# Performance work log

Hardware: AMD Instinct MI355X
Metric: run time of the kernel (lower is better)

## Reference

```python
import jax, jax.numpy as jnp
import numpy as np

D = 64          # graph size d
HID = 1024      # hidden_dim of drift/diffusion MLPs


def _mlp(A_flat, t_val, W1, b1, W2, b2):
    """MLP over flattened adjacency concatenated with scalar time. A_flat: (..., d*d)."""
    t_col = jnp.full(A_flat.shape[:-1] + (1,), t_val, dtype=A_flat.dtype)
    x = jnp.concatenate([A_flat, t_col], axis=-1)          # (..., d*d+1)
    h = jnp.tanh(x @ W1 + b1)                              # (..., HID)
    return h @ W2 + b2                                     # (..., d*d)


def setup_inputs() -> dict:
    key = jax.random.key(0)
    ks = jax.random.split(key, 12)
    B, T = 64, 64
    A0 = jax.random.normal(ks[0], (B, D, D), dtype=jnp.float32)
    t = jnp.arange(T, dtype=jnp.float32) * 0.01
    din = D * D + 1
    s1 = 1.0 / np.sqrt(din)
    s2 = 1.0 / np.sqrt(HID)
    W1f = jax.random.normal(ks[1], (din, HID), jnp.float32) * s1
    b1f = jnp.zeros((HID,), jnp.float32)
    W2f = jax.random.normal(ks[2], (HID, D * D), jnp.float32) * s2
    b2f = jnp.zeros((D * D,), jnp.float32)
    W1g = jax.random.normal(ks[3], (din, HID), jnp.float32) * s1
    b1g = jnp.zeros((HID,), jnp.float32)
    W2g = jax.random.normal(ks[4], (HID, D * D), jnp.float32) * s2
    b2g = jnp.zeros((D * D,), jnp.float32)
    return dict(A0=A0, t=t, W1f=W1f, b1f=b1f, W2f=W2f, b2f=b2f,
                W1g=W1g, b1g=b1g, W2g=W2g, b2g=b2g, num_samples=4)


def reference(A0, t, W1f, b1f, W2f, b2f, W1g, b1g, W2g, b2g, num_samples):
    S = num_samples
    B = A0.shape[0]
    T = t.shape[0]
    dt = t[1] - t[0]
    sqrt_dt = jnp.sqrt(dt)
    A_init = jnp.broadcast_to(A0[None], (S, B, D, D))
    noise_keys = jax.random.split(jax.random.key(42), T - 1)

    def step(A_prev, inp):
        t_prev, k = inp
        Af = A_prev.reshape(S, B, D * D)
        drift = _mlp(Af, t_prev, W1f, b1f, W2f, b2f).reshape(S, B, D, D)
        diffusion = jax.nn.softplus(_mlp(Af, t_prev, W1g, b1g, W2g, b2g)).reshape(S, B, D, D)
        # torch draws dW with shape (*batch, d, d): shared across num_samples
        dW = jax.random.normal(k, (B, D, D), dtype=A_prev.dtype) * sqrt_dt
        A_next = A_prev + drift * dt + diffusion * dW
        return A_next, A_next

    _, traj = jax.lax.scan(step, A_init, (t[:-1], noise_keys))   # (T-1, S, B, d, d)
    A = jnp.concatenate([A_init[None], traj], axis=0)            # (T, S, B, d, d)
    A = jnp.swapaxes(A, 0, 1)                                    # (S, T, B, d, d)
    # ThresholdedSigmoid in training mode + zeroed diagonal
    G = jax.nn.sigmoid(A) * (1.0 - jnp.eye(D, dtype=A.dtype))
    return G
```

## Files before the change

kernel.cpp:

```cpp
#include <hip/hip_runtime.h>
#include <cstdint>

using u16 = unsigned short;
using u32 = uint32_t;
using u64 = unsigned long long;

typedef __bf16 bf16x8 __attribute__((ext_vector_type(8)));
typedef float  f32x4  __attribute__((ext_vector_type(4)));
typedef u32    uvec4  __attribute__((ext_vector_type(4)));

typedef const __attribute__((address_space(1))) void GV;
typedef __attribute__((address_space(3))) void LV;

#define MFMA(a, b, c) __builtin_amdgcn_mfma_f32_16x16x32_bf16((a), (b), (c), 0, 0, 0)
#define SCOPE_AGT __HIP_MEMORY_SCOPE_AGENT

static __device__ __forceinline__ void gl_lds16(const u16* g, u16* l) {
  __builtin_amdgcn_global_load_lds((GV*)g, (LV*)l, 16, 0, 0);
}
static __device__ __forceinline__ void st_dev(u64* p, u64 v) {
  __hip_atomic_store(p, v, __ATOMIC_RELAXED, SCOPE_AGT);
}
static __device__ __forceinline__ void wait_tags(const u32* ctr, int base, u32 tag) {
  const int lane = threadIdx.x & 63;
  const u32* p = ctr + (size_t)(base + (lane & 31)) * 32;
  u32 v = __hip_atomic_load(p, __ATOMIC_RELAXED, SCOPE_AGT);
  while (!__all(v >= tag)) {
    __builtin_amdgcn_s_sleep(4);
    v = __hip_atomic_load(p, __ATOMIC_RELAXED, SCOPE_AGT);
  }
  asm volatile("" ::: "memory");
}

static __device__ __forceinline__ u16 f2bf(float x) {
  u32 u = __float_as_uint(x);
  u32 r = (u + 0x7FFFu + ((u >> 16) & 1u)) >> 16;
  return (u16)r;
}

static __device__ __forceinline__ u32 rotl32(u32 v, int s) {
  return (v << s) | (v >> (32 - s));
}

static __device__ __forceinline__ void threefry2x32(u32 k0, u32 k1, u32 x0, u32 x1,
                                                    u32& o0, u32& o1) {
  u32 k2 = k0 ^ k1 ^ 0x1BD11BDAu;
  x0 += k0; x1 += k1;
  x0 += x1; x1 = rotl32(x1, 13); x1 ^= x0;
  x0 += x1; x1 = rotl32(x1, 15); x1 ^= x0;
  x0 += x1; x1 = rotl32(x1, 26); x1 ^= x0;
  x0 += x1; x1 = rotl32(x1, 6);  x1 ^= x0;
  x0 += k1; x1 += k2 + 1u;
  x0 += x1; x1 = rotl32(x1, 17); x1 ^= x0;
  x0 += x1; x1 = rotl32(x1, 29); x1 ^= x0;
  x0 += x1; x1 = rotl32(x1, 16); x1 ^= x0;
  x0 += x1; x1 = rotl32(x1, 24); x1 ^= x0;
  x0 += k2; x1 += k0 + 2u;
  x0 += x1; x1 = rotl32(x1, 13); x1 ^= x0;
  x0 += x1; x1 = rotl32(x1, 15); x1 ^= x0;
  x0 += x1; x1 = rotl32(x1, 26); x1 ^= x0;
  x0 += x1; x1 = rotl32(x1, 6);  x1 ^= x0;
  x0 += k0; x1 += k1 + 3u;
  x0 += x1; x1 = rotl32(x1, 17); x1 ^= x0;
  x0 += x1; x1 = rotl32(x1, 29); x1 ^= x0;
  x0 += x1; x1 = rotl32(x1, 16); x1 ^= x0;
  x0 += x1; x1 = rotl32(x1, 24); x1 ^= x0;
  x0 += k1; x1 += k2 + 4u;
  x0 += x1; x1 = rotl32(x1, 13); x1 ^= x0;
  x0 += x1; x1 = rotl32(x1, 15); x1 ^= x0;
  x0 += x1; x1 = rotl32(x1, 26); x1 ^= x0;
  x0 += x1; x1 = rotl32(x1, 6);  x1 ^= x0;
  x0 += k2; x1 += k0 + 5u;
  o0 = x0; o1 = x1;
}

static __device__ __forceinline__ float bits_to_normal(u32 bits) {
  const float lo = __uint_as_float(0xBF7FFFFFu);
  float f = __uint_as_float((bits >> 9) | 0x3F800000u) - 1.0f;
  float x = fmaxf(lo, f * 2.0f + lo);
  float w = -logf((1.0f - x) * (1.0f + x));
  float p;
  if (w < 5.0f) {
    w -= 2.5f;
    p = 2.81022636e-08f;
    p = fmaf(p, w, 3.43273939e-07f);
    p = fmaf(p, w, -3.5233877e-06f);
    p = fmaf(p, w, -4.39150654e-06f);
    p = fmaf(p, w, 0.00021858087f);
    p = fmaf(p, w, -0.00125372503f);
    p = fmaf(p, w, -0.00417768164f);
    p = fmaf(p, w, 0.246640727f);
    p = fmaf(p, w, 1.50140941f);
  } else {
    w = sqrtf(w) - 3.0f;
    p = -0.000200214257f;
    p = fmaf(p, w, 0.000100950558f);
    p = fmaf(p, w, 0.00134934322f);
    p = fmaf(p, w, -0.00367342844f);
    p = fmaf(p, w, 0.00573950773f);
    p = fmaf(p, w, -0.0076224613f);
    p = fmaf(p, w, 0.00943887047f);
    p = fmaf(p, w, 1.00167406f);
    p = fmaf(p, w, 2.83297682f);
  }
  return 1.41421356f * p * x;
}

__global__ __launch_bounds__(256) void s1_frag(
    const float* __restrict__ W1f, const float* __restrict__ W1g,
    const float* __restrict__ W2f, const float* __restrict__ W2g,
    u16* __restrict__ W1P, u16* __restrict__ W2P) {
  const int gid = blockIdx.x * 256 + threadIdx.x;
  const int f = gid >> 6, l = gid & 63;
  const int lr = l & 15, kg = l >> 4;
  u32 wbuf[4];
  if (f < 16384) {
    const int net = f >> 13, r = f & 8191, ct = r >> 7, q = r & 127;
    const float* __restrict__ src = net ? W1g : W1f;
    const int k = q * 32 + kg * 8, c = ct * 16 + lr;
    #pragma unroll
    for (int p = 0; p < 4; ++p) {
      u16 e0 = f2bf(src[(size_t)(k + 2 * p) * 1024 + c]);
      u16 e1 = f2bf(src[(size_t)(k + 2 * p + 1) * 1024 + c]);
      wbuf[p] = (u32)e0 | ((u32)e1 << 16);
    }
    *(uvec4*)(W1P + (size_t)f * 512 + l * 8) = *(uvec4*)wbuf;
  } else {
    const int f2 = f - 16384;
    const int net = f2 >> 13, r = f2 & 8191, ct = r >> 5, q = r & 31;
    const float* __restrict__ src = net ? W2g : W2f;
    const int k = q * 32 + kg * 8, c = ct * 16 + lr;
    #pragma unroll
    for (int p = 0; p < 4; ++p) {
      u16 e0 = f2bf(src[(size_t)(k + 2 * p) * 4096 + c]);
      u16 e1 = f2bf(src[(size_t)(k + 2 * p + 1) * 4096 + c]);
      wbuf[p] = (u32)e0 | ((u32)e1 << 16);
    }
    *(uvec4*)(W2P + (size_t)f2 * 512 + l * 8) = *(uvec4*)wbuf;
  }
}

__global__ __launch_bounds__(256) void s2_init(
    const float* __restrict__ A0, u16* __restrict__ APack,
    u32* __restrict__ ctr, float* __restrict__ out) {
  const int gid = blockIdx.x * 256 + threadIdx.x;
  const int n = gid & 4095, b = gid >> 12;
  const float a0 = A0[gid];
  const float sig = (n % 65 == 0) ? 0.0f : 1.0f / (1.0f + expf(-a0));
  #pragma unroll
  for (int s = 0; s < 4; ++s)
    out[((size_t)(s * 64) * 64 + b) * 4096 + n] = sig;
  if (gid < 32768) {
    const int fr = gid >> 6, l = gid & 63;
    const int m = fr >> 7, q = fr & 127;
    const int row = m * 16 + (l & 15);
    const int k = q * 32 + (l >> 4) * 8;
    u32 wbuf[4];
    #pragma unroll
    for (int p = 0; p < 4; ++p) {
      u16 e0 = f2bf(A0[(size_t)row * 4096 + k + 2 * p]);
      u16 e1 = f2bf(A0[(size_t)row * 4096 + k + 2 * p + 1]);
      wbuf[p] = (u32)e0 | ((u32)e1 << 16);
    }
    *(uvec4*)(APack + (size_t)fr * 512 + l * 8) = *(uvec4*)wbuf;
  }
  if (gid < 16640) ctr[gid] = 0;
}

__global__ __launch_bounds__(512, 2) void sde_fused(
    const float* __restrict__ A0, const float* __restrict__ tarr,
    const u16* __restrict__ W1P, const u16* __restrict__ W2P,
    const float* __restrict__ b1f, const float* __restrict__ b1g,
    const float* __restrict__ W1fv, const float* __restrict__ W1gv,
    const float* __restrict__ b2f, const float* __restrict__ b2g,
    u16* __restrict__ APack, u16* __restrict__ HPack,
    u32* __restrict__ ctr, float* __restrict__ out) {
  extern __shared__ __align__(16) char smraw[];
  u16* w2l = (u16*)smraw;
  char* exraw = smraw + 131072;
  f32x4 (*paex)[64]     = (f32x4 (*)[64])exraw;
  u16 (*patile)[16][16] = (u16 (*)[16][16])(exraw + 8192);
  f32x4 (*pbex)[64][2]  = (f32x4 (*)[64][2])exraw;
  u16 (*pbtile)[16][32] = (u16 (*)[16][32])(exraw + 16384);
  uint2* dwk = (uint2*)(exraw + 18432);

  const int bid = blockIdx.x, tix = threadIdx.x;
  const int wid = tix >> 6, lane = tix & 63;
  const int lr = lane & 15, lq = lane >> 4;
  const int mp = bid >> 7;
  const int ctF = bid & 127;
  const int netA = ctF >> 6, ctA = ctF & 63;
  const int mA = wid & 1, ksA = wid >> 1;
  const int mGA = mp * 2 + mA;
  const int ct32 = bid & 127;
  const int ksB = wid >> 2, netB = (wid >> 1) & 1, mB = wid & 1;
  const int mGB = mp * 2 + mB;
  const int eM = wid & 1, eCf = (wid >> 1) & 1, eRh = wid >> 2;
  const int nc = ct32 * 32 + eCf * 16 + lr;

  u32* tagA = ctr + (size_t)bid * 32;
  u32* tagB = ctr + (size_t)(256 + bid) * 32;
  const int waitAbase = 256 + mp * 128 + ksA * 32;
  const int waitBbase = mp * 128 + netB * 64 + ksB * 32;

  #pragma unroll
  for (int i = 0; i < 16; ++i) {
    const int f = wid * 16 + i;
    const int nf = f >> 6, cf = (f >> 5) & 1, ksf = (f >> 4) & 1, df = f & 15;
    const u16* src = W2P
        + ((size_t)((nf * 256 + ct32 * 2 + cf) * 32 + ksf * 16 + df)) * 512 + lane * 8;
    gl_lds16(src, w2l + (size_t)f * 512);
  }
  if (tix < 63) {
    u32 y0, y1;
    threefry2x32(0u, 42u, 0u, (u32)tix, y0, y1);
    dwk[tix] = make_uint2(y0, y1);
  }
  bf16x8 wv[32];
  {
    const u16* pw = W1P + ((size_t)((netA * 64 + ctA) * 128 + ksA * 32)) * 512 + lane * 8;
    #pragma unroll
    for (int d = 0; d < 32; ++d) wv[d] = *(const bf16x8*)(pw + (size_t)d * 512);
  }
  float Ast[2];
  #pragma unroll
  for (int ri = 0; ri < 2; ++ri) {
    const int row = mp * 32 + eM * 16 + lq * 4 + eRh * 2 + ri;
    Ast[ri] = A0[(size_t)row * 4096 + nc];
  }
  const int nclA = ctA * 16 + lr;
  const float bAc = (netA ? b1g : b1f)[nclA];
  const float wAc = ((netA ? W1gv : W1fv) + (size_t)4096 * 1024)[nclA];
  const float bfv = b2f[nc], bgv = b2g[nc];
  const bool diag0 = (nc % 65 == 0);
  asm volatile("s_waitcnt vmcnt(0)" ::: "memory");
  __syncthreads();

  const float dt = tarr[1] - tarr[0];
  const float sdt = sqrtf(dt);

  for (int step = 0; step < 63; ++step) {
    const u32 tag = (u32)step + 1u;
    {
      wait_tags(ctr, waitAbase, (u32)step);
      const u16* pa = APack + (size_t)step * 262144
                    + ((size_t)(mGA * 128 + ksA * 32)) * 512 + lane * 8;
      bf16x8 av[16];
      #pragma unroll
      for (int d = 0; d < 16; ++d) av[d] = *(const bf16x8*)(pa + (size_t)d * 512);
      f32x4 acc0 = {0.f, 0.f, 0.f, 0.f}, acc1 = acc0;
      #pragma unroll
      for (int j = 0; j < 32; ++j) {
        const int s = j & 15;
        if (j & 1) acc1 = MFMA(av[s], wv[j], acc1);
        else       acc0 = MFMA(av[s], wv[j], acc0);
        if (j + 16 < 32) av[s] = *(const bf16x8*)(pa + (size_t)(j + 16) * 512);
      }
      paex[wid][lane] = acc0 + acc1;
      __syncthreads();
      {
        const int gM = wid & 1, gR = wid >> 1;
        const f32x4 s0 = paex[gM][lane];
        const f32x4 s1 = paex[2 + gM][lane];
        const f32x4 s2 = paex[4 + gM][lane];
        const f32x4 s3 = paex[6 + gM][lane];
        const float ch = s0[gR] + s1[gR] + s2[gR] + s3[gR];
        const float cc = bAc + tarr[step] * wAc;
        patile[gM][lq * 4 + gR][lr] = f2bf(tanhf(ch + cc));
      }
      __syncthreads();
      if (wid < 2 && lane < 32) {
        const int mm = wid;
        const int row = lane & 15, kp = lane >> 4;
        const u16* src = &patile[mm][row][kp * 8];
        const u64 lo = *(const u64*)src;
        const u64 hi = *(const u64*)(src + 4);
        const int k8 = (ctA & 1) * 2 + kp;
        u16* dst = HPack + (size_t)step * 131072
                 + ((size_t)((netA * 4 + mp * 2 + mm) * 32 + (ctA >> 1))) * 512
                 + (k8 * 16 + row) * 8;
        st_dev((u64*)dst, lo);
        st_dev((u64*)dst + 1, hi);
      }
      asm volatile("s_waitcnt vmcnt(0)" ::: "memory");
      __syncthreads();
      if (tix == 0)
        __hip_atomic_store(tagA, tag, __ATOMIC_RELAXED, SCOPE_AGT);
    }

    {
      wait_tags(ctr, waitBbase, tag);
      const u16* ph = HPack + (size_t)step * 131072
                    + ((size_t)((netB * 4 + mGB) * 32 + ksB * 16)) * 512 + lane * 8;
      bf16x8 hv[16];
      #pragma unroll
      for (int d = 0; d < 16; ++d) hv[d] = *(const bf16x8*)(ph + (size_t)d * 512);
      const u16* wl0 = w2l + (size_t)(netB * 64 + ksB * 16) * 512 + lane * 8;
      const u16* wl1 = wl0 + (size_t)32 * 512;
      f32x4 a0 = {0.f, 0.f, 0.f, 0.f}, a1 = a0;
      #pragma unroll
      for (int j = 0; j < 16; ++j) {
        const bf16x8 w0 = *(const bf16x8*)(wl0 + (size_t)j * 512);
        const bf16x8 w1 = *(const bf16x8*)(wl1 + (size_t)j * 512);
        a0 = MFMA(hv[j], w0, a0);
        a1 = MFMA(hv[j], w1, a1);
      }
      pbex[wid][lane][0] = a0;
      pbex[wid][lane][1] = a1;
      __syncthreads();
      float sg[2];
      {
        const f32x4 CF = pbex[eM][lane][eCf] + pbex[4 + eM][lane][eCf];
        const f32x4 CG = pbex[2 + eM][lane][eCf] + pbex[6 + eM][lane][eCf];
        const uint2 key = dwk[step];
        #pragma unroll
        for (int ri = 0; ri < 2; ++ri) {
          const int r = eRh * 2 + ri;
          const int row = mp * 32 + eM * 16 + lq * 4 + r;
          const float drift = CF[r] + bfv;
          const float graw = CG[r] + bgv;
          const float diff = fmaxf(graw, 0.0f) + log1pf(expf(-fabsf(graw)));
          u32 y0, y1;
          threefry2x32(key.x, key.y, 0u, (u32)(row * 4096 + nc), y0, y1);
          const float dw = bits_to_normal(y0 ^ y1) * sdt;
          const float an = Ast[ri] + drift * dt + diff * dw;
          Ast[ri] = an;
          pbtile[eM][lq * 4 + r][eCf * 16 + lr] = f2bf(an);
          sg[ri] = diag0 ? 0.0f : 1.0f / (1.0f + expf(-an));
        }
      }
      __syncthreads();
      if (wid < 2) {
        const int mm = wid;
        const int row = lane & 15, kq = lane >> 4;
        const u16* src = &pbtile[mm][row][kq * 8];
        const u64 lo = *(const u64*)src;
        const u64 hi = *(const u64*)(src + 4);
        u16* dst = APack + (size_t)(step + 1) * 262144
                 + ((size_t)((mp * 2 + mm) * 128 + ct32)) * 512 + lane * 8;
        st_dev((u64*)dst, lo);
        st_dev((u64*)dst + 1, hi);
      }
      asm volatile("s_waitcnt vmcnt(0)" ::: "memory");
      __syncthreads();
      if (tix == 0)
        __hip_atomic_store(tagB, tag, __ATOMIC_RELAXED, SCOPE_AGT);
      #pragma unroll
      for (int ri = 0; ri < 2; ++ri) {
        const int row = mp * 32 + eM * 16 + lq * 4 + eRh * 2 + ri;
        #pragma unroll
        for (int s = 0; s < 4; ++s)
          __builtin_nontemporal_store(
              sg[ri], &out[((size_t)(s * 64 + step + 1) * 64 + row) * 4096 + nc]);
      }
    }
  }
}

extern "C" void kernel_launch(void* const* d_in, const int* in_sizes, int n_in,
                              void* d_out, int out_size, void* d_ws, size_t ws_size,
                              hipStream_t stream) {
  const float* A0 = (const float*)d_in[0];
  const float* tarr = (const float*)d_in[1];
  const float* W1f = (const float*)d_in[2];
  const float* b1f = (const float*)d_in[3];
  const float* W2f = (const float*)d_in[4];
  const float* b2f = (const float*)d_in[5];
  const float* W1g = (const float*)d_in[6];
  const float* b1g = (const float*)d_in[7];
  const float* W2g = (const float*)d_in[8];
  const float* b2g = (const float*)d_in[9];
  float* outp = (float*)d_out;
  char* ws = (char*)d_ws;
  const size_t MB = 1024 * 1024;
  u16* W1P   = (u16*)(ws + 0 * MB);
  u16* W2P   = (u16*)(ws + 16 * MB);
  u16* APack = (u16*)(ws + 32 * MB);
  u16* HPack = (u16*)(ws + 64 * MB);
  u32* ctr   = (u32*)(ws + 80 * MB);

  s1_frag<<<dim3(8192), 256, 0, stream>>>(W1f, W1g, W2f, W2g, W1P, W2P);
  s2_init<<<dim3(1024), 256, 0, stream>>>(A0, APack, ctr, outp);

  void* kargs[] = {
    (void*)&A0, (void*)&tarr,
    (void*)&W1P, (void*)&W2P,
    (void*)&b1f, (void*)&b1g, (void*)&W1f, (void*)&W1g,
    (void*)&b2f, (void*)&b2g,
    (void*)&APack, (void*)&HPack, (void*)&ctr, (void*)&outp
  };
  hipLaunchCooperativeKernel((const void*)sde_fused, dim3(256), dim3(512),
                             kargs, 150016, stream);
}
```

Measured before the change: 724.4 us.

## Precompute Brownian noise in a separate kernel and use fast transcendentals

Adds a dw_gen kernel that generates all noise increments with threefry into workspace ahead of the fused solver. Each step prefetches its dw values before waiting on the inter-block tags, which takes the RNG off the serial critical path. The change also replaces tanhf, softplus and sigmoid with exp/rcp approximations, caches the time array in LDS, shortens the spin-wait sleep, and moves the sigmoid after the tag release. In exchange it adds an extra kernel launch and about 64 MB of noise traffic, and the path only runs when the workspace is large enough.

```diff
diff --git a/kernel.cpp b/kernel.cpp
--- a/kernel.cpp
+++ b/kernel.cpp
@@ -26,10 +26,20 @@
   const u32* p = ctr + (size_t)(base + (lane & 31)) * 32;
   u32 v = __hip_atomic_load(p, __ATOMIC_RELAXED, SCOPE_AGT);
   while (!__all(v >= tag)) {
-    __builtin_amdgcn_s_sleep(4);
+    __builtin_amdgcn_s_sleep(1);
     v = __hip_atomic_load(p, __ATOMIC_RELAXED, SCOPE_AGT);
   }
   asm volatile("" ::: "memory");
+}
+
+static __device__ __forceinline__ float tanh_fast(float x) {
+  return 1.0f - 2.0f * __builtin_amdgcn_rcpf(1.0f + __expf(2.0f * x));
+}
+static __device__ __forceinline__ float softplus_fast(float x) {
+  return fmaxf(x, 0.0f) + __logf(1.0f + __expf(-fabsf(x)));
+}
+static __device__ __forceinline__ float sigmoid_fast(float x) {
+  return __builtin_amdgcn_rcpf(1.0f + __expf(-x));
 }
 
 static __device__ __forceinline__ u16 f2bf(float x) {
@@ -167,6 +177,23 @@
   if (gid < 16640) ctr[gid] = 0;
 }
 
+__global__ __launch_bounds__(256) void dw_gen(
+    const float* __restrict__ tarr, float* __restrict__ dst_base) {
+  const int bid = blockIdx.x, tix = threadIdx.x;
+  const int step = bid >> 5, sub = bid & 31;
+  u32 k0, k1;
+  threefry2x32(0u, 42u, 0u, (u32)step, k0, k1);
+  const float sdt = sqrtf(tarr[1] - tarr[0]);
+  float* dst = dst_base + (size_t)step * 262144;
+  #pragma unroll
+  for (int j = 0; j < 32; ++j) {
+    u32 e = (u32)(sub * 8192 + j * 256 + tix);
+    u32 y0, y1;
+    threefry2x32(k0, k1, 0u, e, y0, y1);
+    dst[e] = bits_to_normal(y0 ^ y1) * sdt;
+  }
+}
+
 __global__ __launch_bounds__(512, 2) void sde_fused(
     const float* __restrict__ A0, const float* __restrict__ tarr,
     const u16* __restrict__ W1P, const u16* __restrict__ W2P,
@@ -174,7 +201,8 @@
     const float* __restrict__ W1fv, const float* __restrict__ W1gv,
     const float* __restrict__ b2f, const float* __restrict__ b2g,
     u16* __restrict__ APack, u16* __restrict__ HPack,
-    u32* __restrict__ ctr, float* __restrict__ out) {
+    u32* __restrict__ ctr, const float* __restrict__ dwall,
+    float* __restrict__ out) {
   extern __shared__ __align__(16) char smraw[];
   u16* w2l = (u16*)smraw;
   char* exraw = smraw + 131072;
@@ -183,6 +211,7 @@
   f32x4 (*pbex)[64][2]  = (f32x4 (*)[64][2])exraw;
   u16 (*pbtile)[16][32] = (u16 (*)[16][32])(exraw + 16384);
   uint2* dwk = (uint2*)(exraw + 18432);
+  float* tarrl = (float*)(exraw + 18944);
 
   const int bid = blockIdx.x, tix = threadIdx.x;
   const int wid = tix >> 6, lane = tix & 63;
@@ -216,6 +245,7 @@
     threefry2x32(0u, 42u, 0u, (u32)tix, y0, y1);
     dwk[tix] = make_uint2(y0, y1);
   }
+  if (tix >= 64 && tix < 127) tarrl[tix - 64] = tarr[tix - 64];
   bf16x8 wv[32];
   {
     const u16* pw = W1P + ((size_t)((netA * 64 + ctA) * 128 + ksA * 32)) * 512 + lane * 8;
@@ -233,6 +263,7 @@
   const float wAc = ((netA ? W1gv : W1fv) + (size_t)4096 * 1024)[nclA];
   const float bfv = b2f[nc], bgv = b2g[nc];
   const bool diag0 = (nc % 65 == 0);
+  const int e0dw = (mp * 32 + eM * 16 + lq * 4 + eRh * 2) * 4096 + nc;
   asm volatile("s_waitcnt vmcnt(0)" ::: "memory");
   __syncthreads();
 
@@ -265,8 +296,8 @@
         const f32x4 s2 = paex[4 + gM][lane];
         const f32x4 s3 = paex[6 + gM][lane];
         const float ch = s0[gR] + s1[gR] + s2[gR] + s3[gR];
-        const float cc = bAc + tarr[step] * wAc;
-        patile[gM][lq * 4 + gR][lr] = f2bf(tanhf(ch + cc));
+        const float cc = bAc + tarrl[step] * wAc;
+        patile[gM][lq * 4 + gR][lr] = f2bf(tanh_fast(ch + cc));
       }
       __syncthreads();
       if (wid < 2 && lane < 32) {
@@ -289,6 +320,11 @@
     }
 
     {
+      float dwv0 = 0.f, dwv1 = 0.f;
+      if (dwall) {
+        dwv0 = dwall[(size_t)step * 262144 + e0dw];
+        dwv1 = dwall[(size_t)step * 262144 + e0dw + 4096];
+      }
       wait_tags(ctr, waitBbase, tag);
       const u16* ph = HPack + (size_t)step * 131072
                     + ((size_t)((netB * 4 + mGB) * 32 + ksB * 16)) * 512 + lane * 8;
@@ -308,25 +344,28 @@
       pbex[wid][lane][0] = a0;
       pbex[wid][lane][1] = a1;
       __syncthreads();
-      float sg[2];
+      float anv[2];
       {
         const f32x4 CF = pbex[eM][lane][eCf] + pbex[4 + eM][lane][eCf];
         const f32x4 CG = pbex[2 + eM][lane][eCf] + pbex[6 + eM][lane][eCf];
-        const uint2 key = dwk[step];
+        uint2 key;
+        if (!dwall) key = dwk[step];
         #pragma unroll
         for (int ri = 0; ri < 2; ++ri) {
           const int r = eRh * 2 + ri;
-          const int row = mp * 32 + eM * 16 + lq * 4 + r;
+          float dwv = ri ? dwv1 : dwv0;
+          if (!dwall) {
+            u32 y0, y1;
+            threefry2x32(key.x, key.y, 0u, (u32)(e0dw + ri * 4096), y0, y1);
+            dwv = bits_to_normal(y0 ^ y1) * sdt;
+          }
           const float drift = CF[r] + bfv;
           const float graw = CG[r] + bgv;
-          const float diff = fmaxf(graw, 0.0f) + log1pf(expf(-fabsf(graw)));
-          u32 y0, y1;
-          threefry2x32(key.x, key.y, 0u, (u32)(row * 4096 + nc), y0, y1);
-          const float dw = bits_to_normal(y0 ^ y1) * sdt;
-          const float an = Ast[ri] + drift * dt + diff * dw;
+          const float diff = softplus_fast(graw);
+          const float an = Ast[ri] + drift * dt + diff * dwv;
           Ast[ri] = an;
+          anv[ri] = an;
           pbtile[eM][lq * 4 + r][eCf * 16 + lr] = f2bf(an);
-          sg[ri] = diag0 ? 0.0f : 1.0f / (1.0f + expf(-an));
         }
       }
       __syncthreads();
@@ -347,11 +386,12 @@
         __hip_atomic_store(tagB, tag, __ATOMIC_RELAXED, SCOPE_AGT);
       #pragma unroll
       for (int ri = 0; ri < 2; ++ri) {
+        const float sg = diag0 ? 0.0f : sigmoid_fast(anv[ri]);
         const int row = mp * 32 + eM * 16 + lq * 4 + eRh * 2 + ri;
         #pragma unroll
         for (int s = 0; s < 4; ++s)
           __builtin_nontemporal_store(
-              sg[ri], &out[((size_t)(s * 64 + step + 1) * 64 + row) * 4096 + nc]);
+              sg, &out[((size_t)(s * 64 + step + 1) * 64 + row) * 4096 + nc]);
       }
     }
   }
@@ -378,16 +418,18 @@
   u16* APack = (u16*)(ws + 32 * MB);
   u16* HPack = (u16*)(ws + 64 * MB);
   u32* ctr   = (u32*)(ws + 80 * MB);
+  float* dwall = (ws_size >= (size_t)145 * MB) ? (float*)(ws + 81 * MB) : nullptr;
 
   s1_frag<<<dim3(8192), 256, 0, stream>>>(W1f, W1g, W2f, W2g, W1P, W2P);
   s2_init<<<dim3(1024), 256, 0, stream>>>(A0, APack, ctr, outp);
+  if (dwall) dw_gen<<<dim3(63 * 32), 256, 0, stream>>>(tarr, dwall);
 
   void* kargs[] = {
     (void*)&A0, (void*)&tarr,
     (void*)&W1P, (void*)&W2P,
     (void*)&b1f, (void*)&b1g, (void*)&W1f, (void*)&W1g,
     (void*)&b2f, (void*)&b2g,
-    (void*)&APack, (void*)&HPack, (void*)&ctr, (void*)&outp
+    (void*)&APack, (void*)&HPack, (void*)&ctr, (void*)&dwall, (void*)&outp
   };
   hipLaunchCooperativeKernel((const void*)sde_fused, dim3(256), dim3(512),
                              kargs, 150016, stream);
```

New measurement: 662.4 us. 1.09x faster.
